# Performance work log

Hardware: AMD Instinct MI355X
Metric: run time of the kernel (lower is better)

The kernel has to match this reference:

```python
import jax, jax.numpy as jnp
import numpy as np

B, L, WD = 4096, 30, 300          # batch of news, title length, word dim
H, AD = 20, 20                    # attention heads, per-head dim
MD = H * AD                       # multi_dim = 400
E, ED = 10, 100                   # entities per news, entity dim
QD = 200                          # query_vector_dim
CAT, CD = 18, 50                  # category vocab / dim
SUB, SD = 300, 50                 # subcategory vocab / dim


def _mha(x, wq, bq, wk, bk, wv, bv):
    # x: [B, L, Din] -> [B, L, MD]; standard multi-head self-attention
    b, l, _ = x.shape
    q = (x @ wq + bq).reshape(b, l, H, AD)
    k = (x @ wk + bk).reshape(b, l, H, AD)
    v = (x @ wv + bv).reshape(b, l, H, AD)
    scores = jnp.einsum('blhd,bmhd->bhlm', q, k) / jnp.sqrt(jnp.asarray(AD, x.dtype))
    attn = jax.nn.softmax(scores, axis=-1)
    out = jnp.einsum('bhlm,bmhd->blhd', attn, v)
    return out.reshape(b, l, MD)


def _layernorm(x, g, b):
    mu = jnp.mean(x, axis=-1, keepdims=True)
    var = jnp.var(x, axis=-1, keepdims=True)
    return (x - mu) / jnp.sqrt(var + 1e-5) * g + b


def _additive(x, w, b, q):
    # x: [B, L, D] -> [B, D]
    scores = jnp.tanh(x @ w + b) @ q            # [B, L]
    alpha = jax.nn.softmax(scores, axis=-1)
    return jnp.einsum('bl,bld->bd', alpha, x)


def setup_inputs() -> dict:
    key = jax.random.key(0)
    ks = iter(jax.random.split(key, 40))
    n = lambda shape, s=0.02: (jax.random.normal(next(ks), shape, dtype=jnp.float32) * s)
    inp = {
        'word_embedding': jax.random.normal(next(ks), (B, L, WD), dtype=jnp.float32),
        'entity_embedding': jax.random.normal(next(ks), (B, E, ED), dtype=jnp.float32),
        'category_index': jax.random.randint(next(ks), (B,), 0, CAT, dtype=jnp.int64 if jax.config.jax_enable_x64 else jnp.int32),
        'subcategory_index': jax.random.randint(next(ks), (B,), 0, SUB, dtype=jnp.int64 if jax.config.jax_enable_x64 else jnp.int32),
        # category / subcategory branches
        'emb_cat': n((CAT, CD), 1.0), 'fc1_w': n((CD, MD)), 'fc1_b': jnp.zeros((MD,), jnp.float32),
        'emb_sub': n((SUB, SD), 1.0), 'fc2_w': n((SD, MD)), 'fc2_b': jnp.zeros((MD,), jnp.float32),
        # word multi-head self-attention
        'wq': n((WD, MD)), 'bq': jnp.zeros((MD,), jnp.float32),
        'wk': n((WD, MD)), 'bk': jnp.zeros((MD,), jnp.float32),
        'wv': n((WD, MD)), 'bv': jnp.zeros((MD,), jnp.float32),
        # shared LayerNorm
        'ln_g': jnp.ones((MD,), jnp.float32), 'ln_b': jnp.zeros((MD,), jnp.float32),
        # word additive attention
        'wa_w': n((MD, QD)), 'wa_b': jnp.zeros((QD,), jnp.float32), 'wa_q': n((QD,), 1.0),
        # entity branch: fc3 + GCN (learnable adjacency over the E entities of a news)
        'fc3_w': n((ED, ED)), 'fc3_b': jnp.zeros((ED,), jnp.float32),
        'gcn_A': n((E, E), 1.0), 'gcn_w': n((ED, MD)), 'gcn_b': jnp.zeros((MD,), jnp.float32),
        'ea_w': n((MD, QD)), 'ea_b': jnp.zeros((QD,), jnp.float32), 'ea_q': n((QD,), 1.0),
        # final news-level additive attention over 4 views
        'na_w': n((MD, QD)), 'na_b': jnp.zeros((QD,), jnp.float32), 'na_q': n((QD,), 1.0),
    }
    return inp


def reference(word_embedding, entity_embedding, category_index, subcategory_index,
              emb_cat, fc1_w, fc1_b, emb_sub, fc2_w, fc2_b,
              wq, bq, wk, bk, wv, bv, ln_g, ln_b,
              wa_w, wa_b, wa_q, fc3_w, fc3_b, gcn_A, gcn_w, gcn_b,
              ea_w, ea_b, ea_q, na_w, na_b, na_q):
    # category / subcategory reps (dropout is identity in eval)
    cat_rep = jnp.tanh(emb_cat[category_index] @ fc1_w + fc1_b)      # [B, MD]
    sub_rep = jnp.tanh(emb_sub[subcategory_index] @ fc2_w + fc2_b)   # [B, MD]
    # word branch
    w = _mha(word_embedding, wq, bq, wk, bk, wv, bv)                 # [B, L, MD]
    w = _layernorm(w, ln_g, ln_b)
    word_rep = jnp.tanh(_additive(w, wa_w, wa_b, wa_q))              # [B, MD]
    # entity branch: fc3 -> intra-news GCN -> shared LayerNorm
    e = jnp.tanh(entity_embedding @ fc3_w + fc3_b)                   # [B, E, ED]
    e = jax.nn.relu(jnp.einsum('ef,bfd->bed', gcn_A, e) @ gcn_w + gcn_b)  # [B, E, MD]
    e = _layernorm(e, ln_g, ln_b)
    ent_rep = jnp.tanh(_additive(e, ea_w, ea_b, ea_q))               # [B, MD]
    # fuse the 4 views with additive attention
    views = jnp.stack([word_rep, ent_rep, cat_rep, sub_rep], axis=1)  # [B, 4, MD]
    news_rep = jnp.tanh(_additive(views, na_w, na_b, na_q))          # [B, MD]
    return news_rep
```

## Files before the change

### kernel.cpp

```cpp
#include <hip/hip_runtime.h>
#include <hip/hip_bf16.h>
#include <math.h>

#define B_  4096
#define L_  30
#define WD_ 300
#define H_  20
#define AD_ 20
#define MD_ 400
#define E_  10
#define ED_ 100
#define QD_ 200
#define CD_ 50
#define SD_ 50

typedef unsigned short ushort_t;
typedef __attribute__((ext_vector_type(8))) short bf16x8_t;
typedef __attribute__((ext_vector_type(4))) float f32x4_t;

#define SX_STR   328
#define QKV_STR  1218
#define OUTB_STR 424
#define SOUT_STR 401
#define P_STR    40
#define WT_K     320
#define WAT_K    416

#define N_WT    (1200 * WT_K)
#define N_WAT   (208 * WAT_K)
#define N_FC3T  (112 * 128)
#define N_GCNT  (400 * 128)
#define N_EAT   (208 * WAT_K)

union FragU {
  unsigned  u[4];
  short     s[8];
  bf16x8_t  h;
};

__device__ __forceinline__ ushort_t f2bf(float f) {
  unsigned u = __builtin_bit_cast(unsigned, f);
  unsigned r = (u + 0x7fffu + ((u >> 16) & 1u)) >> 16;
  return (ushort_t)r;
}
__device__ __forceinline__ float bf2f(ushort_t h) {
  return __builtin_bit_cast(float, ((unsigned)h) << 16);
}
__device__ __forceinline__ float wave_reduce_sum(float v) {
  #pragma unroll
  for (int off = 32; off > 0; off >>= 1) v += __shfl_xor(v, off);
  return v;
}
__device__ __forceinline__ void split2(float v, ushort_t* __restrict__ H,
                                       ushort_t* __restrict__ Lo, int idx) {
  const ushort_t h = f2bf(v);
  H[idx] = h;
  Lo[idx] = f2bf(v - bf2f(h));
}

__global__ __launch_bounds__(256) void prep_weights(
    const float* __restrict__ wq, const float* __restrict__ wk, const float* __restrict__ wv,
    const float* __restrict__ wa_w, const float* __restrict__ fc3_w,
    const float* __restrict__ gcn_w, const float* __restrict__ ea_w,
    ushort_t* __restrict__ Wt, ushort_t* __restrict__ Wat,
    ushort_t* __restrict__ fc3TH, ushort_t* __restrict__ fc3TL,
    ushort_t* __restrict__ gcnTH, ushort_t* __restrict__ gcnTL,
    ushort_t* __restrict__ eaTH, ushort_t* __restrict__ eaTL)
{
  int idx = blockIdx.x * 256 + threadIdx.x;
  if (idx < N_WT) {
    const int n = idx / WT_K, k = idx - n * WT_K;
    float v = 0.f;
    if (k < WD_) {
      const float* w = (n < 400) ? wq : (n < 800) ? wk : wv;
      const int c = (n < 400) ? n : (n < 800) ? n - 400 : n - 800;
      v = w[k * MD_ + c];
    }
    Wt[idx] = f2bf(v);
    return;
  }
  idx -= N_WT;
  if (idx < N_WAT) {
    const int q = idx / WAT_K, d = idx - q * WAT_K;
    Wat[idx] = (q < QD_ && d < MD_) ? f2bf(wa_w[d * QD_ + q]) : (ushort_t)0;
    return;
  }
  idx -= N_WAT;
  if (idx < N_FC3T) {
    const int n = idx / 128, k = idx - n * 128;
    const float v = (n < ED_ && k < ED_) ? fc3_w[k * ED_ + n] : 0.f;
    split2(v, fc3TH, fc3TL, idx);
    return;
  }
  idx -= N_FC3T;
  if (idx < N_GCNT) {
    const int n = idx / 128, k = idx - n * 128;
    const float v = (k < ED_) ? gcn_w[k * MD_ + n] : 0.f;
    split2(v, gcnTH, gcnTL, idx);
    return;
  }
  idx -= N_GCNT;
  if (idx < N_EAT) {
    const int q = idx / WAT_K, d = idx - q * WAT_K;
    const float v = (q < QD_ && d < MD_) ? ea_w[d * QD_ + q] : 0.f;
    split2(v, eaTH, eaTL, idx);
  }
}

__global__ __launch_bounds__(1024, 4) void word_branch_kernel(
    const float* __restrict__ X,
    const ushort_t* __restrict__ Wt, const ushort_t* __restrict__ Wat,
    const float* __restrict__ bq, const float* __restrict__ bk, const float* __restrict__ bv,
    const float* __restrict__ ln_g, const float* __restrict__ ln_b,
    const float* __restrict__ wa_b, const float* __restrict__ wa_q,
    float* __restrict__ word_rep)
{
  __shared__ __align__(16) union {
    ushort_t x[32 * SX_STR];
    ushort_t p[16 * 32 * P_STR];
  } uA;
  __shared__ __align__(16) union {
    ushort_t qkv[30 * QKV_STR];
    ushort_t o[32 * OUTB_STR];
  } uB;
  __shared__ __align__(16) float sOut[30 * SOUT_STR];
  __shared__ float sSc[32];
  __shared__ float sAlpha[32];

  const int b    = blockIdx.x;
  const int tid  = threadIdx.x;
  const int wave = tid >> 6;
  const int lane = tid & 63;
  const int lr   = lane & 15;
  const int kg   = lane >> 4;

  const float* xb = X + (size_t)b * (L_ * WD_);
  {
    const int r = tid >> 5;
    const int c0 = tid & 31;
    #pragma unroll
    for (int k = 0; k < 10; ++k) {
      const int c = c0 + k * 32;
      const float v = (r < L_ && c < WD_) ? xb[r * WD_ + c] : 0.f;
      uA.x[r * SX_STR + c] = f2bf(v);
    }
  }
  if (tid < 32) sSc[tid] = 0.f;
  __syncthreads();

  for (int jt = wave; jt < 38; jt += 16) {
    const int nt0 = 2 * jt, nt1 = 2 * jt + 1;
    const bool has1 = (nt1 < 75);
    f32x4_t a00 = {0,0,0,0}, a10 = {0,0,0,0}, a01 = {0,0,0,0}, a11 = {0,0,0,0};
    for (int ks = 0; ks < 10; ++ks) {
      const int kb = ks * 32 + kg * 8;
      bf16x8_t af0 = *reinterpret_cast<const bf16x8_t*>(&uA.x[lr * SX_STR + kb]);
      bf16x8_t af1 = *reinterpret_cast<const bf16x8_t*>(&uA.x[(16 + lr) * SX_STR + kb]);
      bf16x8_t bf0 = *reinterpret_cast<const bf16x8_t*>(&Wt[(nt0 * 16 + lr) * WT_K + kb]);
      a00 = __builtin_amdgcn_mfma_f32_16x16x32_bf16(af0, bf0, a00, 0, 0, 0);
      a10 = __builtin_amdgcn_mfma_f32_16x16x32_bf16(af1, bf0, a10, 0, 0, 0);
      if (has1) {
        bf16x8_t bf1 = *reinterpret_cast<const bf16x8_t*>(&Wt[(nt1 * 16 + lr) * WT_K + kb]);
        a01 = __builtin_amdgcn_mfma_f32_16x16x32_bf16(af0, bf1, a01, 0, 0, 0);
        a11 = __builtin_amdgcn_mfma_f32_16x16x32_bf16(af1, bf1, a11, 0, 0, 0);
      }
    }
    #pragma unroll
    for (int half = 0; half < 2; ++half) {
      if (half && !has1) break;
      const int nt = half ? nt1 : nt0;
      const int col = nt * 16 + lr;
      const float bias = (col < 400) ? bq[col] : (col < 800) ? bk[col - 400] : bv[col - 800];
      const f32x4_t am0 = half ? a01 : a00;
      const f32x4_t am1 = half ? a11 : a10;
      #pragma unroll
      for (int i = 0; i < 4; ++i) {
        uB.qkv[(kg * 4 + i) * QKV_STR + col] = f2bf(am0[i] + bias);
        const int r2 = 16 + kg * 4 + i;
        if (r2 < L_) uB.qkv[r2 * QKV_STR + col] = f2bf(am1[i] + bias);
      }
    }
  }
  __syncthreads();

  ushort_t* pw = &uA.p[wave * (32 * P_STR)];
  for (int h = wave; h < H_; h += 16) {
    const int hq = h * AD_, hk = 400 + h * AD_, hv = 800 + h * AD_;

    bf16x8_t aq[2], bkf[2];
    #pragma unroll
    for (int t = 0; t < 2; ++t) {
      FragU fq, fk;
      fq.u[0]=fq.u[1]=fq.u[2]=fq.u[3]=0;
      fk.u[0]=fk.u[1]=fk.u[2]=fk.u[3]=0;
      const bool okrow = (t == 0) || (lr < 14);
      if (okrow && kg < 3) {
        const ushort_t* pq = &uB.qkv[(t * 16 + lr) * QKV_STR + hq + kg * 8];
        const ushort_t* pk = &uB.qkv[(t * 16 + lr) * QKV_STR + hk + kg * 8];
        fq.u[0] = *(const unsigned*)(pq);     fq.u[1] = *(const unsigned*)(pq + 2);
        fk.u[0] = *(const unsigned*)(pk);     fk.u[1] = *(const unsigned*)(pk + 2);
        if (kg < 2) {
          fq.u[2] = *(const unsigned*)(pq + 4); fq.u[3] = *(const unsigned*)(pq + 6);
          fk.u[2] = *(const unsigned*)(pk + 4); fk.u[3] = *(const unsigned*)(pk + 6);
        }
      }
      aq[t] = fq.h; bkf[t] = fk.h;
    }
    f32x4_t c00 = {0,0,0,0}, c01 = {0,0,0,0}, c10 = {0,0,0,0}, c11 = {0,0,0,0};
    c00 = __builtin_amdgcn_mfma_f32_16x16x32_bf16(aq[0], bkf[0], c00, 0, 0, 0);
    c01 = __builtin_amdgcn_mfma_f32_16x16x32_bf16(aq[0], bkf[1], c01, 0, 0, 0);
    c10 = __builtin_amdgcn_mfma_f32_16x16x32_bf16(aq[1], bkf[0], c10, 0, 0, 0);
    c11 = __builtin_amdgcn_mfma_f32_16x16x32_bf16(aq[1], bkf[1], c11, 0, 0, 0);

    const float SCALE = 0.2236067977499790f;
    #pragma unroll
    for (int mt = 0; mt < 2; ++mt) {
      const f32x4_t v0f = mt ? c10 : c00;
      const f32x4_t v1f = mt ? c11 : c01;
      #pragma unroll
      for (int i = 0; i < 4; ++i) {
        const float v0 = v0f[i] * SCALE;
        const float v1 = (lr < 14) ? v1f[i] * SCALE : -1e30f;
        float mx = fmaxf(v0, v1);
        mx = fmaxf(mx, __shfl_xor(mx, 1));
        mx = fmaxf(mx, __shfl_xor(mx, 2));
        mx = fmaxf(mx, __shfl_xor(mx, 4));
        mx = fmaxf(mx, __shfl_xor(mx, 8));
        const float e0 = __expf(v0 - mx);
        const float e1 = (lr < 14) ? __expf(v1 - mx) : 0.f;
        float s = e0 + e1;
        s += __shfl_xor(s, 1);
        s += __shfl_xor(s, 2);
        s += __shfl_xor(s, 4);
        s += __shfl_xor(s, 8);
        const float inv = 1.f / s;
        const int row = mt * 16 + kg * 4 + i;
        pw[row * P_STR + lr]      = f2bf(e0 * inv);
        pw[row * P_STR + 16 + lr] = f2bf(e1 * inv);
      }
    }
    __asm__ volatile("s_waitcnt lgkmcnt(0)" ::: "memory");

    bf16x8_t ap[2];
    ap[0] = *reinterpret_cast<const bf16x8_t*>(&pw[lr * P_STR + kg * 8]);
    ap[1] = *reinterpret_cast<const bf16x8_t*>(&pw[(16 + lr) * P_STR + kg * 8]);
    bf16x8_t bvf[2];
    #pragma unroll
    for (int nt = 0; nt < 2; ++nt) {
      FragU f;
      const int d = nt * 16 + lr;
      if (d < AD_) {
        #pragma unroll
        for (int j = 0; j < 8; ++j) {
          const int rm = kg * 8 + j;
          f.s[j] = (rm < L_) ? (short)uB.qkv[rm * QKV_STR + hv + d] : (short)0;
        }
      } else {
        f.u[0]=f.u[1]=f.u[2]=f.u[3]=0;
      }
      bvf[nt] = f.h;
    }
    f32x4_t o00 = {0,0,0,0}, o01 = {0,0,0,0}, o10 = {0,0,0,0}, o11 = {0,0,0,0};
    o00 = __builtin_amdgcn_mfma_f32_16x16x32_bf16(ap[0], bvf[0], o00, 0, 0, 0);
    o01 = __builtin_amdgcn_mfma_f32_16x16x32_bf16(ap[0], bvf[1], o01, 0, 0, 0);
    o10 = __builtin_amdgcn_mfma_f32_16x16x32_bf16(ap[1], bvf[0], o10, 0, 0, 0);
    o11 = __builtin_amdgcn_mfma_f32_16x16x32_bf16(ap[1], bvf[1], o11, 0, 0, 0);

    #pragma unroll
    for (int mt = 0; mt < 2; ++mt) {
      #pragma unroll
      for (int nt = 0; nt < 2; ++nt) {
        const f32x4_t o = mt ? (nt ? o11 : o10) : (nt ? o01 : o00);
        const int d = nt * 16 + lr;
        if (d < AD_) {
          #pragma unroll
          for (int i = 0; i < 4; ++i) {
            const int r = mt * 16 + kg * 4 + i;
            if (r < L_) sOut[r * SOUT_STR + h * AD_ + d] = o[i];
          }
        }
      }
    }
  }
  __syncthreads();

  for (int r = wave; r < L_; r += 16) {
    float s = 0.f, s2 = 0.f;
    for (int d = lane; d < MD_; d += 64) { const float v = sOut[r * SOUT_STR + d]; s += v; s2 += v * v; }
    s  = wave_reduce_sum(s);
    s2 = wave_reduce_sum(s2);
    const float mu  = s * (1.f / MD_);
    const float var = s2 * (1.f / MD_) - mu * mu;
    const float inv = rsqrtf(var + 1e-5f);
    for (int d = lane; d < MD_; d += 64)
      sOut[r * SOUT_STR + d] = (sOut[r * SOUT_STR + d] - mu) * inv * ln_g[d] + ln_b[d];
  }
  __syncthreads();

  {
    const int r = tid >> 5;
    const int c0 = tid & 31;
    #pragma unroll
    for (int k = 0; k < 13; ++k) {
      const int c = c0 + k * 32;
      if (c < 416) {
        const float v = (r < L_ && c < MD_) ? sOut[r * SOUT_STR + c] : 0.f;
        uB.o[r * OUTB_STR + c] = f2bf(v);
      }
    }
  }
  __syncthreads();

  for (int t = wave; t < 26; t += 16) {
    const int mt = t & 1, nt = t >> 1;
    f32x4_t acc = {0,0,0,0};
    for (int ks = 0; ks < 13; ++ks) {
      const int kb = ks * 32 + kg * 8;
      bf16x8_t af = *reinterpret_cast<const bf16x8_t*>(&uB.o[(mt * 16 + lr) * OUTB_STR + kb]);
      bf16x8_t wf = *reinterpret_cast<const bf16x8_t*>(&Wat[(nt * 16 + lr) * WAT_K + kb]);
      acc = __builtin_amdgcn_mfma_f32_16x16x32_bf16(af, wf, acc, 0, 0, 0);
    }
    const int q = nt * 16 + lr;
    if (q < QD_) {
      const float bb = wa_b[q], qq = wa_q[q];
      #pragma unroll
      for (int i = 0; i < 4; ++i) {
        const int row = mt * 16 + kg * 4 + i;
        if (row < L_) atomicAdd(&sSc[row], tanhf(acc[i] + bb) * qq);
      }
    }
  }
  __syncthreads();

  if (wave == 0) {
    const float v = (lane < L_) ? sSc[lane] : -1e30f;
    float mx = v;
    #pragma unroll
    for (int off = 32; off > 0; off >>= 1) mx = fmaxf(mx, __shfl_xor(mx, off));
    const float e = (lane < L_) ? __expf(v - mx) : 0.f;
    float s = e;
    #pragma unroll
    for (int off = 32; off > 0; off >>= 1) s += __shfl_xor(s, off);
    if (lane < L_) sAlpha[lane] = e / s;
  }
  __syncthreads();

  if (tid < MD_) {
    const int d = tid;
    float acc = 0.f;
    #pragma unroll 6
    for (int l = 0; l < L_; ++l) acc += sAlpha[l] * sOut[l * SOUT_STR + d];
    word_rep[(size_t)b * MD_ + d] = tanhf(acc);
  }
}

__global__ __launch_bounds__(512, 4) void entity_branch_kernel(
    const float* __restrict__ Ein,
    const ushort_t* __restrict__ fc3TH, const ushort_t* __restrict__ fc3TL,
    const float* __restrict__ fc3_b,
    const float* __restrict__ gcn_A,
    const ushort_t* __restrict__ gcnTH, const ushort_t* __restrict__ gcnTL,
    const float* __restrict__ gcn_b,
    const float* __restrict__ ln_g, const float* __restrict__ ln_b,
    const ushort_t* __restrict__ eaTH, const ushort_t* __restrict__ eaTL,
    const float* __restrict__ ea_b, const float* __restrict__ ea_q,
    float* __restrict__ ent_rep)
{
  __shared__ __align__(16) ushort_t sEh[16 * 136], sEl[16 * 136];
  __shared__ __align__(16) float    eF[E_ * 104];
  __shared__ __align__(16) ushort_t gH[16 * 136], gL[16 * 136];
  __shared__ __align__(16) float    sR[16 * SOUT_STR];
  __shared__ __align__(16) ushort_t oH[16 * OUTB_STR], oL[16 * OUTB_STR];
  __shared__ float sSc[16];
  __shared__ float sAlpha[16];

  const int b    = blockIdx.x;
  const int tid  = threadIdx.x;
  const int wave = tid >> 6;
  const int lane = tid & 63;
  const int lr   = lane & 15;
  const int kg   = lane >> 4;

  for (int id = tid; id < 16 * 128; id += 512) {
    const int r = id >> 7, c = id & 127;
    const float v = (r < E_ && c < ED_) ? Ein[(size_t)b * (E_ * ED_) + r * ED_ + c] : 0.f;
    const ushort_t hh = f2bf(v);
    sEh[r * 136 + c] = hh;
    sEl[r * 136 + c] = f2bf(v - bf2f(hh));
  }
  for (int id = tid; id < 16 * 136; id += 512) { gH[id] = 0; gL[id] = 0; }
  if (tid < 16) sSc[tid] = 0.f;
  __syncthreads();

  for (int nt = wave; nt < 7; nt += 8) {
    f32x4_t acc = {0,0,0,0};
    #pragma unroll
    for (int ks = 0; ks < 4; ++ks) {
      const int kb = ks * 32 + kg * 8;
      bf16x8_t ah = *reinterpret_cast<const bf16x8_t*>(&sEh[lr * 136 + kb]);
      bf16x8_t al = *reinterpret_cast<const bf16x8_t*>(&sEl[lr * 136 + kb]);
      bf16x8_t wh = *reinterpret_cast<const bf16x8_t*>(&fc3TH[(nt * 16 + lr) * 128 + kb]);
      bf16x8_t wl = *reinterpret_cast<const bf16x8_t*>(&fc3TL[(nt * 16 + lr) * 128 + kb]);
      acc = __builtin_amdgcn_mfma_f32_16x16x32_bf16(ah, wh, acc, 0, 0, 0);
      acc = __builtin_amdgcn_mfma_f32_16x16x32_bf16(al, wh, acc, 0, 0, 0);
      acc = __builtin_amdgcn_mfma_f32_16x16x32_bf16(ah, wl, acc, 0, 0, 0);
    }
    const int d = nt * 16 + lr;
    if (d < ED_) {
      const float bias = fc3_b[d];
      #pragma unroll
      for (int i = 0; i < 4; ++i) {
        const int r = kg * 4 + i;
        if (r < E_) eF[r * 104 + d] = tanhf(acc[i] + bias);
      }
    }
  }
  __syncthreads();

  for (int id = tid; id < E_ * ED_; id += 512) {
    const int i = id / ED_, d = id - (id / ED_) * ED_;
    float acc = 0.f;
    #pragma unroll
    for (int f = 0; f < E_; ++f) acc += gcn_A[i * E_ + f] * eF[f * 104 + d];
    const ushort_t hh = f2bf(acc);
    gH[i * 136 + d] = hh;
    gL[i * 136 + d] = f2bf(acc - bf2f(hh));
  }
  __syncthreads();

  for (int nt = wave; nt < 25; nt += 8) {
    f32x4_t acc = {0,0,0,0};
    #pragma unroll
    for (int ks = 0; ks < 4; ++ks) {
      const int kb = ks * 32 + kg * 8;
      bf16x8_t ah = *reinterpret_cast<const bf16x8_t*>(&gH[lr * 136 + kb]);
      bf16x8_t al = *reinterpret_cast<const bf16x8_t*>(&gL[lr * 136 + kb]);
      bf16x8_t wh = *reinterpret_cast<const bf16x8_t*>(&gcnTH[(nt * 16 + lr) * 128 + kb]);
      bf16x8_t wl = *reinterpret_cast<const bf16x8_t*>(&gcnTL[(nt * 16 + lr) * 128 + kb]);
      acc = __builtin_amdgcn_mfma_f32_16x16x32_bf16(ah, wh, acc, 0, 0, 0);
      acc = __builtin_amdgcn_mfma_f32_16x16x32_bf16(al, wh, acc, 0, 0, 0);
      acc = __builtin_amdgcn_mfma_f32_16x16x32_bf16(ah, wl, acc, 0, 0, 0);
    }
    const int d = nt * 16 + lr;
    const float bias = gcn_b[d];
    #pragma unroll
    for (int i = 0; i < 4; ++i) {
      const int r = kg * 4 + i;
      if (r < E_) sR[r * SOUT_STR + d] = fmaxf(acc[i] + bias, 0.f);
    }
  }
  __syncthreads();

  for (int r = wave; r < E_; r += 8) {
    float s = 0.f, s2 = 0.f;
    for (int d = lane; d < MD_; d += 64) { const float v = sR[r * SOUT_STR + d]; s += v; s2 += v * v; }
    s  = wave_reduce_sum(s);
    s2 = wave_reduce_sum(s2);
    const float mu  = s * (1.f / MD_);
    const float var = s2 * (1.f / MD_) - mu * mu;
    const float inv = rsqrtf(var + 1e-5f);
    for (int d = lane; d < MD_; d += 64)
      sR[r * SOUT_STR + d] = (sR[r * SOUT_STR + d] - mu) * inv * ln_g[d] + ln_b[d];
  }
  __syncthreads();

  {
    const int r = tid >> 5;
    const int c0 = tid & 31;
    #pragma unroll
    for (int k = 0; k < 13; ++k) {
      const int c = c0 + k * 32;
      const float v = (r < E_ && c < MD_) ? sR[r * SOUT_STR + c] : 0.f;
      const ushort_t hh = f2bf(v);
      oH[r * OUTB_STR + c] = hh;
      oL[r * OUTB_STR + c] = f2bf(v - bf2f(hh));
    }
  }
  __syncthreads();

  for (int nt = wave; nt < 13; nt += 8) {
    f32x4_t acc = {0,0,0,0};
    for (int ks = 0; ks < 13; ++ks) {
      const int kb = ks * 32 + kg * 8;
      bf16x8_t ah = *reinterpret_cast<const bf16x8_t*>(&oH[lr * OUTB_STR + kb]);
      bf16x8_t al = *reinterpret_cast<const bf16x8_t*>(&oL[lr * OUTB_STR + kb]);
      bf16x8_t wh = *reinterpret_cast<const bf16x8_t*>(&eaTH[(nt * 16 + lr) * WAT_K + kb]);
      bf16x8_t wl = *reinterpret_cast<const bf16x8_t*>(&eaTL[(nt * 16 + lr) * WAT_K + kb]);
      acc = __builtin_amdgcn_mfma_f32_16x16x32_bf16(ah, wh, acc, 0, 0, 0);
      acc = __builtin_amdgcn_mfma_f32_16x16x32_bf16(al, wh, acc, 0, 0, 0);
      acc = __builtin_amdgcn_mfma_f32_16x16x32_bf16(ah, wl, acc, 0, 0, 0);
    }
    const int q = nt * 16 + lr;
    if (q < QD_) {
      const float bb = ea_b[q], qq = ea_q[q];
      #pragma unroll
      for (int i = 0; i < 4; ++i) {
        const int r = kg * 4 + i;
        if (r < E_) atomicAdd(&sSc[r], tanhf(acc[i] + bb) * qq);
      }
    }
  }
  __syncthreads();

  if (wave == 0) {
    const float v = (lane < E_) ? sSc[lane] : -1e30f;
    float mx = v;
    #pragma unroll
    for (int off = 32; off > 0; off >>= 1) mx = fmaxf(mx, __shfl_xor(mx, off));
    const float e = (lane < E_) ? __expf(v - mx) : 0.f;
    float s = e;
    #pragma unroll
    for (int off = 32; off > 0; off >>= 1) s += __shfl_xor(s, off);
    if (lane < E_) sAlpha[lane] = e / s;
  }
  __syncthreads();

  if (tid < MD_) {
    const int d = tid;
    float acc = 0.f;
    #pragma unroll
    for (int i = 0; i < E_; ++i) acc += sAlpha[i] * sR[i * SOUT_STR + d];
    ent_rep[(size_t)b * MD_ + d] = tanhf(acc);
  }
}

__global__ __launch_bounds__(256) void catsub_kernel(
    const int* __restrict__ cat_idx, const int* __restrict__ sub_idx,
    const float* __restrict__ emb_cat, const float* __restrict__ fc1_w, const float* __restrict__ fc1_b,
    const float* __restrict__ emb_sub, const float* __restrict__ fc2_w, const float* __restrict__ fc2_b,
    float* __restrict__ cat_rep, float* __restrict__ sub_rep)
{
  int idx = blockIdx.x * 256 + threadIdx.x;
  const int total = B_ * MD_;
  if (idx < total) {
    const int b = idx / MD_, d = idx - (idx / MD_) * MD_;
    const float* row = emb_cat + (size_t)cat_idx[b] * CD_;
    float acc = fc1_b[d];
    #pragma unroll
    for (int k = 0; k < CD_; ++k) acc += row[k] * fc1_w[k * MD_ + d];
    cat_rep[idx] = tanhf(acc);
  } else {
    idx -= total;
    if (idx < total) {
      const int b = idx / MD_, d = idx - (idx / MD_) * MD_;
      const float* row = emb_sub + (size_t)sub_idx[b] * SD_;
      float acc = fc2_b[d];
      #pragma unroll
      for (int k = 0; k < SD_; ++k) acc += row[k] * fc2_w[k * MD_ + d];
      sub_rep[idx] = tanhf(acc);
    }
  }
}

__global__ __launch_bounds__(256) void fuse_kernel(
    const float* __restrict__ word_rep, const float* __restrict__ ent_rep,
    const float* __restrict__ cat_rep, const float* __restrict__ sub_rep,
    const float* __restrict__ na_w, const float* __restrict__ na_b, const float* __restrict__ na_q,
    float* __restrict__ out)
{
  __shared__ float sViews[4][MD_];
  __shared__ float sSc[4];
  __shared__ float sAlpha[4];
  const int b = blockIdx.x, tid = threadIdx.x;
  for (int d = tid; d < MD_; d += 256) {
    sViews[0][d] = word_rep[(size_t)b * MD_ + d];
    sViews[1][d] = ent_rep[(size_t)b * MD_ + d];
    sViews[2][d] = cat_rep[(size_t)b * MD_ + d];
    sViews[3][d] = sub_rep[(size_t)b * MD_ + d];
  }
  if (tid < 4) sSc[tid] = 0.f;
  __syncthreads();
  for (int id = tid; id < 4 * QD_; id += 256) {
    const int v = id / QD_, q = id - (id / QD_) * QD_;
    float acc = na_b[q];
    #pragma unroll 4
    for (int d = 0; d < MD_; ++d) acc += sViews[v][d] * na_w[d * QD_ + q];
    atomicAdd(&sSc[v], tanhf(acc) * na_q[q]);
  }
  __syncthreads();
  if (tid == 0) {
    float mx = -1e30f;
    for (int v = 0; v < 4; ++v) mx = fmaxf(mx, sSc[v]);
    float sum = 0.f;
    for (int v = 0; v < 4; ++v) { const float e = __expf(sSc[v] - mx); sAlpha[v] = e; sum += e; }
    const float inv = 1.f / sum;
    for (int v = 0; v < 4; ++v) sAlpha[v] *= inv;
  }
  __syncthreads();
  for (int d = tid; d < MD_; d += 256) {
    const float acc = sAlpha[0] * sViews[0][d] + sAlpha[1] * sViews[1][d] +
                      sAlpha[2] * sViews[2][d] + sAlpha[3] * sViews[3][d];
    out[(size_t)b * MD_ + d] = tanhf(acc);
  }
}

extern "C" void kernel_launch(void* const* d_in, const int* in_sizes, int n_in,
                              void* d_out, int out_size, void* d_ws, size_t ws_size,
                              hipStream_t stream) {
  const float* X        = (const float*)d_in[0];
  const float* Ein      = (const float*)d_in[1];
  const int*   cat_idx  = (const int*)d_in[2];
  const int*   sub_idx  = (const int*)d_in[3];
  const float* emb_cat  = (const float*)d_in[4];
  const float* fc1_w    = (const float*)d_in[5];
  const float* fc1_b    = (const float*)d_in[6];
  const float* emb_sub  = (const float*)d_in[7];
  const float* fc2_w    = (const float*)d_in[8];
  const float* fc2_b    = (const float*)d_in[9];
  const float* wq       = (const float*)d_in[10];
  const float* bq       = (const float*)d_in[11];
  const float* wk       = (const float*)d_in[12];
  const float* bk       = (const float*)d_in[13];
  const float* wv       = (const float*)d_in[14];
  const float* bv       = (const float*)d_in[15];
  const float* ln_g     = (const float*)d_in[16];
  const float* ln_b     = (const float*)d_in[17];
  const float* wa_w     = (const float*)d_in[18];
  const float* wa_b     = (const float*)d_in[19];
  const float* wa_q     = (const float*)d_in[20];
  const float* fc3_w    = (const float*)d_in[21];
  const float* fc3_b    = (const float*)d_in[22];
  const float* gcn_A    = (const float*)d_in[23];
  const float* gcn_w    = (const float*)d_in[24];
  const float* gcn_b    = (const float*)d_in[25];
  const float* ea_w     = (const float*)d_in[26];
  const float* ea_b     = (const float*)d_in[27];
  const float* ea_q     = (const float*)d_in[28];
  const float* na_w     = (const float*)d_in[29];
  const float* na_b     = (const float*)d_in[30];
  const float* na_q     = (const float*)d_in[31];

  float* out = (float*)d_out;
  const size_t BM = (size_t)B_ * MD_;
  float* word_rep = (float*)d_ws;
  float* ent_rep  = word_rep + BM;
  float* cat_rep  = ent_rep + BM;
  float* sub_rep  = cat_rep + BM;
  ushort_t* Wt    = (ushort_t*)(sub_rep + BM);
  ushort_t* Wat   = Wt + N_WT;
  ushort_t* fc3TH = Wat + N_WAT;
  ushort_t* fc3TL = fc3TH + N_FC3T;
  ushort_t* gcnTH = fc3TL + N_FC3T;
  ushort_t* gcnTL = gcnTH + N_GCNT;
  ushort_t* eaTH  = gcnTL + N_GCNT;
  ushort_t* eaTL  = eaTH + N_EAT;

  {
    const int total = N_WT + N_WAT + N_FC3T + N_GCNT + N_EAT;
    prep_weights<<<(total + 255) / 256, 256, 0, stream>>>(
        wq, wk, wv, wa_w, fc3_w, gcn_w, ea_w,
        Wt, Wat, fc3TH, fc3TL, gcnTH, gcnTL, eaTH, eaTL);
  }
  word_branch_kernel<<<B_, 1024, 0, stream>>>(X, Wt, Wat, bq, bk, bv,
                                              ln_g, ln_b, wa_b, wa_q, word_rep);
  entity_branch_kernel<<<B_, 512, 0, stream>>>(Ein, fc3TH, fc3TL, fc3_b, gcn_A,
                                               gcnTH, gcnTL, gcn_b,
                                               ln_g, ln_b, eaTH, eaTL, ea_b, ea_q, ent_rep);
  catsub_kernel<<<(2 * B_ * MD_) / 256, 256, 0, stream>>>(cat_idx, sub_idx,
                                                          emb_cat, fc1_w, fc1_b,
                                                          emb_sub, fc2_w, fc2_b,
                                                          cat_rep, sub_rep);
  fuse_kernel<<<B_, 256, 0, stream>>>(word_rep, ent_rep, cat_rep, sub_rep,
                                      na_w, na_b, na_q, out);
}
```

Before: 1.326 ms.

## Rebalance wave work in word branch and prefetch weight fragments into registers

The QKV projection loop now gives each wave one 16-column tile over 75 tiles instead of pairs over 38, and all ten weight fragments are preloaded into registers before the MFMA chain. The attention loop is split into 40 (head, row-half) units instead of 20 heads, so all 16 waves get work, which halves the per-wave softmax scratch in LDS. The additive-attention projection likewise preloads its 13 weight fragments. The aim is better load balance across waves and hiding global weight-load latency, at the cost of more registers and fewer B-fragment reuses per A load.

Result: no change. 1.323 ms (-0.3%).

```diff
diff --git a/kernel.cpp b/kernel.cpp
--- a/kernel.cpp
+++ b/kernel.cpp
@@ -117,7 +117,7 @@
 {
   __shared__ __align__(16) union {
     ushort_t x[32 * SX_STR];
-    ushort_t p[16 * 32 * P_STR];
+    ushort_t p[16 * 16 * P_STR];
   } uA;
   __shared__ __align__(16) union {
     ushort_t qkv[30 * QKV_STR];
@@ -148,102 +148,90 @@
   if (tid < 32) sSc[tid] = 0.f;
   __syncthreads();
 
-  for (int jt = wave; jt < 38; jt += 16) {
-    const int nt0 = 2 * jt, nt1 = 2 * jt + 1;
-    const bool has1 = (nt1 < 75);
-    f32x4_t a00 = {0,0,0,0}, a10 = {0,0,0,0}, a01 = {0,0,0,0}, a11 = {0,0,0,0};
+  for (int nt = wave; nt < 75; nt += 16) {
+    const ushort_t* wbase = &Wt[(nt * 16 + lr) * WT_K + kg * 8];
+    bf16x8_t bfa[10];
+    #pragma unroll
+    for (int ks = 0; ks < 10; ++ks)
+      bfa[ks] = *reinterpret_cast<const bf16x8_t*>(wbase + ks * 32);
+    f32x4_t acc0 = {0,0,0,0}, acc1 = {0,0,0,0};
+    #pragma unroll
     for (int ks = 0; ks < 10; ++ks) {
       const int kb = ks * 32 + kg * 8;
       bf16x8_t af0 = *reinterpret_cast<const bf16x8_t*>(&uA.x[lr * SX_STR + kb]);
       bf16x8_t af1 = *reinterpret_cast<const bf16x8_t*>(&uA.x[(16 + lr) * SX_STR + kb]);
-      bf16x8_t bf0 = *reinterpret_cast<const bf16x8_t*>(&Wt[(nt0 * 16 + lr) * WT_K + kb]);
-      a00 = __builtin_amdgcn_mfma_f32_16x16x32_bf16(af0, bf0, a00, 0, 0, 0);
-      a10 = __builtin_amdgcn_mfma_f32_16x16x32_bf16(af1, bf0, a10, 0, 0, 0);
-      if (has1) {
-        bf16x8_t bf1 = *reinterpret_cast<const bf16x8_t*>(&Wt[(nt1 * 16 + lr) * WT_K + kb]);
-        a01 = __builtin_amdgcn_mfma_f32_16x16x32_bf16(af0, bf1, a01, 0, 0, 0);
-        a11 = __builtin_amdgcn_mfma_f32_16x16x32_bf16(af1, bf1, a11, 0, 0, 0);
-      }
-    }
-    #pragma unroll
-    for (int half = 0; half < 2; ++half) {
-      if (half && !has1) break;
-      const int nt = half ? nt1 : nt0;
-      const int col = nt * 16 + lr;
-      const float bias = (col < 400) ? bq[col] : (col < 800) ? bk[col - 400] : bv[col - 800];
-      const f32x4_t am0 = half ? a01 : a00;
-      const f32x4_t am1 = half ? a11 : a10;
-      #pragma unroll
-      for (int i = 0; i < 4; ++i) {
-        uB.qkv[(kg * 4 + i) * QKV_STR + col] = f2bf(am0[i] + bias);
-        const int r2 = 16 + kg * 4 + i;
-        if (r2 < L_) uB.qkv[r2 * QKV_STR + col] = f2bf(am1[i] + bias);
-      }
-    }
-  }
-  __syncthreads();
-
-  ushort_t* pw = &uA.p[wave * (32 * P_STR)];
-  for (int h = wave; h < H_; h += 16) {
+      acc0 = __builtin_amdgcn_mfma_f32_16x16x32_bf16(af0, bfa[ks], acc0, 0, 0, 0);
+      acc1 = __builtin_amdgcn_mfma_f32_16x16x32_bf16(af1, bfa[ks], acc1, 0, 0, 0);
+    }
+    const int col = nt * 16 + lr;
+    const float bias = (col < 400) ? bq[col] : (col < 800) ? bk[col - 400] : bv[col - 800];
+    #pragma unroll
+    for (int i = 0; i < 4; ++i) {
+      uB.qkv[(kg * 4 + i) * QKV_STR + col] = f2bf(acc0[i] + bias);
+      const int r2 = 16 + kg * 4 + i;
+      if (r2 < L_) uB.qkv[r2 * QKV_STR + col] = f2bf(acc1[i] + bias);
+    }
+  }
+  __syncthreads();
+
+  ushort_t* pw = &uA.p[wave * (16 * P_STR)];
+  for (int u = wave; u < 2 * H_; u += 16) {
+    const int h = u >> 1, mt = u & 1;
     const int hq = h * AD_, hk = 400 + h * AD_, hv = 800 + h * AD_;
 
-    bf16x8_t aq[2], bkf[2];
+    bf16x8_t aq, bkf[2];
+    {
+      FragU fq;
+      fq.u[0]=fq.u[1]=fq.u[2]=fq.u[3]=0;
+      const bool okrow = (mt == 0) || (lr < 14);
+      if (okrow && kg < 3) {
+        const ushort_t* pq = &uB.qkv[(mt * 16 + lr) * QKV_STR + hq + kg * 8];
+        fq.u[0] = *(const unsigned*)(pq);     fq.u[1] = *(const unsigned*)(pq + 2);
+        if (kg < 2) { fq.u[2] = *(const unsigned*)(pq + 4); fq.u[3] = *(const unsigned*)(pq + 6); }
+      }
+      aq = fq.h;
+    }
     #pragma unroll
     for (int t = 0; t < 2; ++t) {
-      FragU fq, fk;
-      fq.u[0]=fq.u[1]=fq.u[2]=fq.u[3]=0;
+      FragU fk;
       fk.u[0]=fk.u[1]=fk.u[2]=fk.u[3]=0;
       const bool okrow = (t == 0) || (lr < 14);
       if (okrow && kg < 3) {
-        const ushort_t* pq = &uB.qkv[(t * 16 + lr) * QKV_STR + hq + kg * 8];
         const ushort_t* pk = &uB.qkv[(t * 16 + lr) * QKV_STR + hk + kg * 8];
-        fq.u[0] = *(const unsigned*)(pq);     fq.u[1] = *(const unsigned*)(pq + 2);
         fk.u[0] = *(const unsigned*)(pk);     fk.u[1] = *(const unsigned*)(pk + 2);
-        if (kg < 2) {
-          fq.u[2] = *(const unsigned*)(pq + 4); fq.u[3] = *(const unsigned*)(pq + 6);
-          fk.u[2] = *(const unsigned*)(pk + 4); fk.u[3] = *(const unsigned*)(pk + 6);
-        }
-      }
-      aq[t] = fq.h; bkf[t] = fk.h;
-    }
-    f32x4_t c00 = {0,0,0,0}, c01 = {0,0,0,0}, c10 = {0,0,0,0}, c11 = {0,0,0,0};
-    c00 = __builtin_amdgcn_mfma_f32_16x16x32_bf16(aq[0], bkf[0], c00, 0, 0, 0);
-    c01 = __builtin_amdgcn_mfma_f32_16x16x32_bf16(aq[0], bkf[1], c01, 0, 0, 0);
-    c10 = __builtin_amdgcn_mfma_f32_16x16x32_bf16(aq[1], bkf[0], c10, 0, 0, 0);
-    c11 = __builtin_amdgcn_mfma_f32_16x16x32_bf16(aq[1], bkf[1], c11, 0, 0, 0);
+        if (kg < 2) { fk.u[2] = *(const unsigned*)(pk + 4); fk.u[3] = *(const unsigned*)(pk + 6); }
+      }
+      bkf[t] = fk.h;
+    }
+    f32x4_t c0 = {0,0,0,0}, c1 = {0,0,0,0};
+    c0 = __builtin_amdgcn_mfma_f32_16x16x32_bf16(aq, bkf[0], c0, 0, 0, 0);
+    c1 = __builtin_amdgcn_mfma_f32_16x16x32_bf16(aq, bkf[1], c1, 0, 0, 0);
 
     const float SCALE = 0.2236067977499790f;
     #pragma unroll
-    for (int mt = 0; mt < 2; ++mt) {
-      const f32x4_t v0f = mt ? c10 : c00;
-      const f32x4_t v1f = mt ? c11 : c01;
-      #pragma unroll
-      for (int i = 0; i < 4; ++i) {
-        const float v0 = v0f[i] * SCALE;
-        const float v1 = (lr < 14) ? v1f[i] * SCALE : -1e30f;
-        float mx = fmaxf(v0, v1);
-        mx = fmaxf(mx, __shfl_xor(mx, 1));
-        mx = fmaxf(mx, __shfl_xor(mx, 2));
-        mx = fmaxf(mx, __shfl_xor(mx, 4));
-        mx = fmaxf(mx, __shfl_xor(mx, 8));
-        const float e0 = __expf(v0 - mx);
-        const float e1 = (lr < 14) ? __expf(v1 - mx) : 0.f;
-        float s = e0 + e1;
-        s += __shfl_xor(s, 1);
-        s += __shfl_xor(s, 2);
-        s += __shfl_xor(s, 4);
-        s += __shfl_xor(s, 8);
-        const float inv = 1.f / s;
-        const int row = mt * 16 + kg * 4 + i;
-        pw[row * P_STR + lr]      = f2bf(e0 * inv);
-        pw[row * P_STR + 16 + lr] = f2bf(e1 * inv);
-      }
+    for (int i = 0; i < 4; ++i) {
+      const float v0 = c0[i] * SCALE;
+      const float v1 = (lr < 14) ? c1[i] * SCALE : -1e30f;
+      float mx = fmaxf(v0, v1);
+      mx = fmaxf(mx, __shfl_xor(mx, 1));
+      mx = fmaxf(mx, __shfl_xor(mx, 2));
+      mx = fmaxf(mx, __shfl_xor(mx, 4));
+      mx = fmaxf(mx, __shfl_xor(mx, 8));
+      const float e0 = __expf(v0 - mx);
+      const float e1 = (lr < 14) ? __expf(v1 - mx) : 0.f;
+      float s = e0 + e1;
+      s += __shfl_xor(s, 1);
+      s += __shfl_xor(s, 2);
+      s += __shfl_xor(s, 4);
+      s += __shfl_xor(s, 8);
+      const float inv = 1.f / s;
+      const int row = kg * 4 + i;
+      pw[row * P_STR + lr]      = f2bf(e0 * inv);
+      pw[row * P_STR + 16 + lr] = f2bf(e1 * inv);
     }
     __asm__ volatile("s_waitcnt lgkmcnt(0)" ::: "memory");
 
-    bf16x8_t ap[2];
-    ap[0] = *reinterpret_cast<const bf16x8_t*>(&pw[lr * P_STR + kg * 8]);
-    ap[1] = *reinterpret_cast<const bf16x8_t*>(&pw[(16 + lr) * P_STR + kg * 8]);
+    bf16x8_t ap = *reinterpret_cast<const bf16x8_t*>(&pw[lr * P_STR + kg * 8]);
     bf16x8_t bvf[2];
     #pragma unroll
     for (int nt = 0; nt < 2; ++nt) {
@@ -260,24 +248,19 @@
       }
       bvf[nt] = f.h;
     }
-    f32x4_t o00 = {0,0,0,0}, o01 = {0,0,0,0}, o10 = {0,0,0,0}, o11 = {0,0,0,0};
-    o00 = __builtin_amdgcn_mfma_f32_16x16x32_bf16(ap[0], bvf[0], o00, 0, 0, 0);
-    o01 = __builtin_amdgcn_mfma_f32_16x16x32_bf16(ap[0], bvf[1], o01, 0, 0, 0);
-    o10 = __builtin_amdgcn_mfma_f32_16x16x32_bf16(ap[1], bvf[0], o10, 0, 0, 0);
-    o11 = __builtin_amdgcn_mfma_f32_16x16x32_bf16(ap[1], bvf[1], o11, 0, 0, 0);
-
-    #pragma unroll
-    for (int mt = 0; mt < 2; ++mt) {
-      #pragma unroll
-      for (int nt = 0; nt < 2; ++nt) {
-        const f32x4_t o = mt ? (nt ? o11 : o10) : (nt ? o01 : o00);
-        const int d = nt * 16 + lr;
-        if (d < AD_) {
-          #pragma unroll
-          for (int i = 0; i < 4; ++i) {
-            const int r = mt * 16 + kg * 4 + i;
-            if (r < L_) sOut[r * SOUT_STR + h * AD_ + d] = o[i];
-          }
+    f32x4_t o0 = {0,0,0,0}, o1 = {0,0,0,0};
+    o0 = __builtin_amdgcn_mfma_f32_16x16x32_bf16(ap, bvf[0], o0, 0, 0, 0);
+    o1 = __builtin_amdgcn_mfma_f32_16x16x32_bf16(ap, bvf[1], o1, 0, 0, 0);
+
+    #pragma unroll
+    for (int nt = 0; nt < 2; ++nt) {
+      const f32x4_t o = nt ? o1 : o0;
+      const int d = nt * 16 + lr;
+      if (d < AD_) {
+        #pragma unroll
+        for (int i = 0; i < 4; ++i) {
+          const int r = mt * 16 + kg * 4 + i;
+          if (r < L_) sOut[r * SOUT_STR + h * AD_ + d] = o[i];
         }
       }
     }
@@ -314,11 +297,16 @@
   for (int t = wave; t < 26; t += 16) {
     const int mt = t & 1, nt = t >> 1;
     f32x4_t acc = {0,0,0,0};
+    const ushort_t* wbase = &Wat[(nt * 16 + lr) * WAT_K + kg * 8];
+    bf16x8_t wfa[13];
+    #pragma unroll
+    for (int ks = 0; ks < 13; ++ks)
+      wfa[ks] = *reinterpret_cast<const bf16x8_t*>(wbase + ks * 32);
+    #pragma unroll
     for (int ks = 0; ks < 13; ++ks) {
       const int kb = ks * 32 + kg * 8;
       bf16x8_t af = *reinterpret_cast<const bf16x8_t*>(&uB.o[(mt * 16 + lr) * OUTB_STR + kb]);
-      bf16x8_t wf = *reinterpret_cast<const bf16x8_t*>(&Wat[(nt * 16 + lr) * WAT_K + kb]);
-      acc = __builtin_amdgcn_mfma_f32_16x16x32_bf16(af, wf, acc, 0, 0, 0);
+      acc = __builtin_amdgcn_mfma_f32_16x16x32_bf16(af, wfa[ks], acc, 0, 0, 0);
     }
     const int q = nt * 16 + lr;
     if (q < QD_) {
```
